# Kernel optimization log

Hardware: AMD Instinct MI355X
Metric: run time of the kernel (lower is better)

Reference implementation:

```python
import jax, jax.numpy as jnp
import numpy as np

EPS = 1e-5
K = 3
N_TAP = K * K


def _bn(x, g, b, m, v):
    # eval-mode batchnorm over channel axis 1 of NCHW
    inv = g / jnp.sqrt(v + EPS)
    return x * inv[None, :, None, None] + (b - m * inv)[None, :, None, None]


def _silu(x):
    return x * jax.nn.sigmoid(x)


def _dcn(x, offset, mask, w, b, pad=1):
    """Modulated deformable conv (DCNv2), stride 1.
    x: [B,C,H,W], offset: [B,2n,H,W] ((dy,dx) per tap), mask: [B,n,H,W],
    w: [O,C,K,K], b: [O]."""
    B, C, H, W = x.shape
    O = w.shape[0]
    ky, kx = jnp.meshgrid(jnp.arange(K), jnp.arange(K), indexing='ij')
    ky = ky.reshape(N_TAP).astype(x.dtype)
    kx = kx.reshape(N_TAP).astype(x.dtype)
    off = offset.reshape(B, N_TAP, 2, H, W)
    base_y = jnp.arange(H, dtype=x.dtype)[None, None, :, None]
    base_x = jnp.arange(W, dtype=x.dtype)[None, None, None, :]
    # fractional sample positions [B,n,H,W]
    py = base_y - pad + ky[None, :, None, None] + off[:, :, 0]
    px = base_x - pad + kx[None, :, None, None] + off[:, :, 1]
    y0 = jnp.floor(py)
    x0 = jnp.floor(px)
    fy = py - y0
    fx = px - x0
    y0i = y0.astype(jnp.int32)
    x0i = x0.astype(jnp.int32)
    x_flat = x.reshape(B, C, 1, H * W)

    def corner(yi, xi, wgt):
        valid = (yi >= 0) & (yi < H) & (xi >= 0) & (xi < W)
        idx = (jnp.clip(yi, 0, H - 1) * W + jnp.clip(xi, 0, W - 1)).reshape(B, 1, N_TAP, H * W)
        v = jnp.take_along_axis(x_flat, idx, axis=-1)  # [B,C,n,HW]
        return v * (wgt * valid.astype(x.dtype)).reshape(B, 1, N_TAP, H * W)

    acc = corner(y0i, x0i, (1 - fy) * (1 - fx))
    acc = acc + corner(y0i, x0i + 1, (1 - fy) * fx)
    acc = acc + corner(y0i + 1, x0i, fy * (1 - fx))
    acc = acc + corner(y0i + 1, x0i + 1, fy * fx)
    val = acc.reshape(B, C, N_TAP, H, W) * mask[:, None]  # modulation
    out = jnp.einsum('bcnhw,ocn->bohw', val, w.reshape(O, C, N_TAP))
    return out + b[None, :, None, None]


def setup_inputs() -> dict:
    key = jax.random.key(0)
    ks = jax.random.split(key, 16)
    B, C1, H, W = 8, 256, 80, 80
    C2 = 256
    Ch = 128  # c_ = int(c2 * 0.5)
    d = {}
    d['x'] = jax.random.normal(ks[0], (B, C1, H, W), jnp.float32)
    # cv1: 1x1 conv (no bias) + BN
    d['cv1_w'] = jax.random.normal(ks[1], (Ch, C1), jnp.float32) * (1.0 / np.sqrt(C1))
    d['bn1_g'] = jax.random.uniform(ks[2], (Ch,), jnp.float32, 0.5, 1.5)
    d['bn1_b'] = jax.random.normal(ks[3], (Ch,), jnp.float32) * 0.1
    d['bn1_m'] = jax.random.normal(ks[4], (Ch,), jnp.float32) * 0.1
    d['bn1_v'] = jax.random.uniform(ks[5], (Ch,), jnp.float32, 0.5, 1.5)
    # offset/mask predictor 3x3 conv (small weights -> modest deformation)
    d['off_w'] = jax.random.normal(ks[6], (3 * N_TAP, Ch, K, K), jnp.float32) * 0.01
    d['off_b'] = jnp.zeros((3 * N_TAP,), jnp.float32)
    # dcn main weight/bias
    d['dcn_w'] = jax.random.normal(ks[7], (Ch, Ch, K, K), jnp.float32) * (1.0 / np.sqrt(Ch * N_TAP))
    d['dcn_b'] = jnp.zeros((Ch,), jnp.float32)
    d['bn2_g'] = jax.random.uniform(ks[8], (Ch,), jnp.float32, 0.5, 1.5)
    d['bn2_b'] = jax.random.normal(ks[9], (Ch,), jnp.float32) * 0.1
    d['bn2_m'] = jax.random.normal(ks[10], (Ch,), jnp.float32) * 0.1
    d['bn2_v'] = jax.random.uniform(ks[11], (Ch,), jnp.float32, 0.5, 1.5)
    # cv2: 1x1 conv (no bias) + BN
    d['cv2_w'] = jax.random.normal(ks[12], (C2, Ch), jnp.float32) * (1.0 / np.sqrt(Ch))
    d['bn3_g'] = jax.random.uniform(ks[13], (C2,), jnp.float32, 0.5, 1.5)
    d['bn3_b'] = jax.random.normal(ks[14], (C2,), jnp.float32) * 0.1
    d['bn3_m'] = jax.random.normal(ks[15], (C2,), jnp.float32) * 0.1
    d['bn3_v'] = jnp.ones((C2,), jnp.float32)
    return d


def reference(x, cv1_w, bn1_g, bn1_b, bn1_m, bn1_v,
              off_w, off_b, dcn_w, dcn_b, bn2_g, bn2_b, bn2_m, bn2_v,
              cv2_w, bn3_g, bn3_b, bn3_m, bn3_v):
    # cv1: 1x1 conv -> BN -> SiLU
    y = _silu(_bn(jnp.einsum('bchw,oc->bohw', x, cv1_w), bn1_g, bn1_b, bn1_m, bn1_v))
    # offset/mask predictor: 3x3 conv, pad 1
    raw = jax.lax.conv_general_dilated(
        y, off_w, window_strides=(1, 1), padding=((1, 1), (1, 1)),
        dimension_numbers=('NCHW', 'OIHW', 'NCHW')) + off_b[None, :, None, None]
    offset = raw[:, :2 * N_TAP]
    mask = jax.nn.sigmoid(raw[:, 2 * N_TAP:])
    # modulated deformable 3x3 conv -> BN -> SiLU
    y = _silu(_bn(_dcn(y, offset, mask, dcn_w, dcn_b), bn2_g, bn2_b, bn2_m, bn2_v))
    # cv2: 1x1 conv -> BN -> SiLU
    y = _silu(_bn(jnp.einsum('bchw,oc->bohw', y, cv2_w), bn3_g, bn3_b, bn3_m, bn3_v))
    return x + y  # shortcut (c1 == c2)
```

## Files before the change

### kernel.cpp

```cpp
#include <hip/hip_runtime.h>
#include <math.h>

#define HWSZ 6400
#define WIMG 80
#define HIMG 80
#define BEPS 1e-5f

typedef __attribute__((ext_vector_type(8))) short short8;
typedef __attribute__((ext_vector_type(4))) float f32x4;

__device__ __forceinline__ unsigned short f2b(float f) {
    unsigned u = __builtin_bit_cast(unsigned, f);
    u += 0x7fffu + ((u >> 16) & 1u);
    return (unsigned short)(u >> 16);
}
__device__ __forceinline__ float b2f(unsigned short h) {
    unsigned u = ((unsigned)h) << 16;
    return __builtin_bit_cast(float, u);
}
__device__ __forceinline__ float silu_f(float t) { return t / (1.f + __expf(-t)); }

#define BPOS(sub, nt, n16, q) (((((sub)*4 + (nt))*16 + (n16))*40) + (q)*8)

__global__ __launch_bounds__(256) void k_prep(
    const float* __restrict__ cv1w, const float* __restrict__ g1, const float* __restrict__ b1,
    const float* __restrict__ m1, const float* __restrict__ v1,
    const float* __restrict__ offw, const float* __restrict__ offb,
    const float* __restrict__ dcnw, const float* __restrict__ dcnb,
    const float* __restrict__ g2, const float* __restrict__ b2,
    const float* __restrict__ m2, const float* __restrict__ v2,
    const float* __restrict__ cv2w, const float* __restrict__ g3, const float* __restrict__ b3,
    const float* __restrict__ m3, const float* __restrict__ v3,
    unsigned short* __restrict__ apk1, unsigned short* __restrict__ apko,
    unsigned short* __restrict__ apkd, unsigned short* __restrict__ apk2,
    float* __restrict__ bias1, float* __restrict__ biaso,
    float* __restrict__ bias2, float* __restrict__ bias3)
{
    int idx = blockIdx.x * 256 + threadIdx.x;
    if (idx < 32768) {
        int j = idx & 7, L = (idx >> 3) & 63, ks = (idx >> 9) & 7, mt = idx >> 12;
        int o = mt * 16 + (L & 15), k = ks * 32 + (L >> 4) * 8 + j;
        float inv = g1[o] * rsqrtf(v1[o] + BEPS);
        apk1[idx] = f2b(cv1w[o * 256 + k] * inv);
    } else if (idx < 69632) {
        int t = idx - 32768;
        int j = t & 7, L = (t >> 3) & 63;
        int mt = t / 18432, rem = t % 18432, ks = rem >> 9;
        int o = mt * 16 + (L & 15);
        int kp = ks * 32 + (L >> 4) * 8 + j;
        int n = kp >> 7, c = kp & 127;
        float wv = (o < 27) ? offw[(size_t)(o * 128 + c) * 9 + n] : 0.f;
        apko[t] = f2b(wv);
    } else if (idx < 217088) {
        int t = idx - 69632;
        int j = t & 7, L = (t >> 3) & 63;
        int mt = t / 18432, rem = t % 18432, ks = rem >> 9;
        int o = mt * 16 + (L & 15);
        int kp = ks * 32 + (L >> 4) * 8 + j;
        int n = kp >> 7, c = kp & 127;
        float inv = g2[o] * rsqrtf(v2[o] + BEPS);
        apkd[t] = f2b(dcnw[(size_t)(o * 128 + c) * 9 + n] * inv);
    } else if (idx < 249856) {
        int t = idx - 217088;
        int j = t & 7, L = (t >> 3) & 63, ks = (t >> 9) & 3, mt = t >> 11;
        int o = mt * 16 + (L & 15), k = ks * 32 + (L >> 4) * 8 + j;
        float inv = g3[o] * rsqrtf(v3[o] + BEPS);
        apk2[t] = f2b(cv2w[o * 128 + k] * inv);
    } else if (idx < 250395) {
        int t = idx - 249856;
        if (t < 128) { float inv = g1[t] * rsqrtf(v1[t] + BEPS); bias1[t] = b1[t] - m1[t] * inv; }
        else if (t < 155) { biaso[t - 128] = offb[t - 128]; }
        else if (t < 283) { int o = t - 155; float inv = g2[o] * rsqrtf(v2[o] + BEPS);
                            bias2[o] = dcnb[o] * inv + b2[o] - m2[o] * inv; }
        else { int o = t - 283; float inv = g3[o] * rsqrtf(v3[o] + BEPS); bias3[o] = b3[o] - m3[o] * inv; }
    }
}

__global__ __launch_bounds__(256) void k_cv1(
    const float* __restrict__ x, const unsigned short* __restrict__ apk1,
    const float* __restrict__ bias1, unsigned short* __restrict__ y1t)
{
    __shared__ __align__(16) unsigned short sB[20480];
    int blk = blockIdx.x;
    int b = blk / 100, pt = blk % 100;
    int p0 = pt * 64;
    int tid = threadIdx.x;
    int lane = tid & 63;
    int w = tid >> 6;
    {
        int px = lane, q = w;
        const float* xb = x + (size_t)b * 256 * HWSZ + p0 + px;
        for (int ks = 0; ks < 8; ++ks) {
            short8 v;
#pragma unroll
            for (int j = 0; j < 8; ++j)
                v[j] = (short)f2b(xb[(size_t)(ks * 32 + q * 8 + j) * HWSZ]);
            *(short8*)&sB[((ks * 4 + (px >> 4)) * 16 + (px & 15)) * 40 + q * 8] = v;
        }
    }
    __syncthreads();
    int n16 = lane & 15, qd = lane >> 4;
    f32x4 acc[2][4];
#pragma unroll
    for (int mi = 0; mi < 2; ++mi)
#pragma unroll
        for (int nt = 0; nt < 4; ++nt) acc[mi][nt] = (f32x4){0.f, 0.f, 0.f, 0.f};
    for (int ks = 0; ks < 8; ++ks) {
        short8 bf[4];
#pragma unroll
        for (int nt = 0; nt < 4; ++nt)
            bf[nt] = *(const short8*)&sB[((ks * 4 + nt) * 16 + n16) * 40 + qd * 8];
#pragma unroll
        for (int mi = 0; mi < 2; ++mi) {
            int mt = w * 2 + mi;
            short8 af = *(const short8*)&apk1[(size_t)((mt * 8 + ks) * 64 + lane) * 8];
#pragma unroll
            for (int nt = 0; nt < 4; ++nt)
                acc[mi][nt] = __builtin_amdgcn_mfma_f32_16x16x32_bf16(af, bf[nt], acc[mi][nt], 0, 0, 0);
        }
    }
    __syncthreads();
#pragma unroll
    for (int mi = 0; mi < 2; ++mi)
#pragma unroll
        for (int nt = 0; nt < 4; ++nt)
#pragma unroll
            for (int r = 0; r < 4; ++r) {
                int o = w * 32 + mi * 16 + qd * 4 + r;
                float sv = silu_f(acc[mi][nt][r] + bias1[o]);
                sB[(nt * 16 + n16) * 136 + o] = f2b(sv);
            }
    __syncthreads();
    {
        int px = tid >> 2, qq = tid & 3;
        unsigned short* ytb = y1t + ((size_t)b * HWSZ + p0 + px) * 128;
#pragma unroll
        for (int seg = 0; seg < 4; ++seg) {
            short8 v = *(const short8*)&sB[px * 136 + qq * 32 + seg * 8];
            *(short8*)&ytb[qq * 32 + seg * 8] = v;
        }
    }
}

__global__ __launch_bounds__(256) void k_off(
    const unsigned short* __restrict__ y1t, const unsigned short* __restrict__ apko,
    const float* __restrict__ biaso, float* __restrict__ raw)
{
    __shared__ __align__(16) unsigned short sV[10240];
    int blk = blockIdx.x;
    int b = blk / 100, pt = blk % 100;
    int p0 = pt * 64;
    int tid = threadIdx.x;
    int lane = tid & 63, w = tid >> 6;
    int n16 = lane & 15, qd = lane >> 4;
    int pxl = tid >> 2, q = tid & 3;
    int p = p0 + pxl;
    int h = p / WIMG, wx = p % WIMG;
    const unsigned short* yb = y1t + (size_t)b * HWSZ * 128;
    f32x4 acc[2];
    acc[0] = (f32x4){0.f, 0.f, 0.f, 0.f};
    acc[1] = (f32x4){0.f, 0.f, 0.f, 0.f};
    const short8 zz = {0, 0, 0, 0, 0, 0, 0, 0};
    for (int n = 0; n < 9; ++n) {
        int hh = h - 1 + n / 3, ww = wx - 1 + n % 3;
        bool valid = ((unsigned)hh < HIMG) && ((unsigned)ww < WIMG);
        int spx = valid ? hh * WIMG + ww : 0;
        const unsigned short* ys = yb + (size_t)spx * 128 + q * 8;
#pragma unroll
        for (int sub = 0; sub < 4; ++sub) {
            short8 v = *(const short8*)&ys[sub * 32];
            if (!valid) v = zz;
            *(short8*)&sV[BPOS(sub, pxl >> 4, pxl & 15, q)] = v;
        }
        __syncthreads();
#pragma unroll
        for (int sub = 0; sub < 4; ++sub) {
            int ks = n * 4 + sub;
            short8 bf = *(const short8*)&sV[BPOS(sub, w, n16, qd)];
#pragma unroll
            for (int mi = 0; mi < 2; ++mi) {
                short8 af = *(const short8*)&apko[(size_t)((mi * 36 + ks) * 64 + lane) * 8];
                acc[mi] = __builtin_amdgcn_mfma_f32_16x16x32_bf16(af, bf, acc[mi], 0, 0, 0);
            }
        }
        __syncthreads();
    }
    float* rb = raw + (size_t)b * 27 * HWSZ + p0 + w * 16 + n16;
#pragma unroll
    for (int mi = 0; mi < 2; ++mi)
#pragma unroll
        for (int r = 0; r < 4; ++r) {
            int o = mi * 16 + qd * 4 + r;
            if (o < 27) {
                float t = acc[mi][r] + biaso[o];
                if (o >= 18) t = 1.f / (1.f + __expf(-t));
                rb[(size_t)o * HWSZ] = t;
            }
        }
}

__global__ __launch_bounds__(256) void k_dcn(
    const unsigned short* __restrict__ y1t, const float* __restrict__ raw,
    const unsigned short* __restrict__ apkd, const float* __restrict__ bias2,
    unsigned short* __restrict__ zt)
{
    __shared__ float swgt[4][9][64];
    __shared__ unsigned short sidx[4][9][64];
    __shared__ __align__(16) unsigned short sV[10240];
    int blk = blockIdx.x;
    int b = blk / 100, pt = blk % 100;
    int p0 = pt * 64;
    int tid = threadIdx.x;

    for (int i = tid; i < 576; i += 256) {
        int n = i / 64, pp = i % 64;
        int p = p0 + pp;
        int h = p / WIMG, wx = p % WIMG;
        const float* rb = raw + (size_t)b * 27 * HWSZ + p;
        float dy = rb[(size_t)(2 * n) * HWSZ];
        float dx = rb[(size_t)(2 * n + 1) * HWSZ];
        float mk = rb[(size_t)(18 + n) * HWSZ];
        float py = (float)(h - 1 + n / 3) + dy;
        float px = (float)(wx - 1 + n % 3) + dx;
        float y0f = floorf(py), x0f = floorf(px);
        float fy = py - y0f, fx = px - x0f;
        int y0 = (int)y0f, x0 = (int)x0f;
#pragma unroll
        for (int k = 0; k < 4; ++k) {
            int yy = y0 + (k >> 1);
            int xx = x0 + (k & 1);
            bool valid = ((unsigned)yy < HIMG) && ((unsigned)xx < WIMG);
            float wk = ((k >> 1) ? fy : 1.f - fy) * ((k & 1) ? fx : 1.f - fx);
            wk = valid ? wk * mk : 0.f;
            int yc = min(max(yy, 0), HIMG - 1);
            int xc = min(max(xx, 0), WIMG - 1);
            sidx[k][n][pp] = (unsigned short)(yc * WIMG + xc);
            swgt[k][n][pp] = wk;
        }
    }
    __syncthreads();

    int lane = tid & 63, w = tid >> 6;
    int n16 = lane & 15, qd = lane >> 4;
    int pxl = tid >> 2, q = tid & 3;
    const unsigned short* yb = y1t + (size_t)b * HWSZ * 128;
    f32x4 acc[2][4];
#pragma unroll
    for (int mi = 0; mi < 2; ++mi)
#pragma unroll
        for (int nt = 0; nt < 4; ++nt) acc[mi][nt] = (f32x4){0.f, 0.f, 0.f, 0.f};

    for (int n = 0; n < 9; ++n) {
        float av[4][8];
#pragma unroll
        for (int sub = 0; sub < 4; ++sub)
#pragma unroll
            for (int j = 0; j < 8; ++j) av[sub][j] = 0.f;
#pragma unroll
        for (int k = 0; k < 4; ++k) {
            float wk = swgt[k][n][pxl];
            const unsigned short* ys = yb + (size_t)sidx[k][n][pxl] * 128 + q * 8;
#pragma unroll
            for (int sub = 0; sub < 4; ++sub) {
                short8 v = *(const short8*)&ys[sub * 32];
#pragma unroll
                for (int j = 0; j < 8; ++j)
                    av[sub][j] = fmaf(wk, b2f((unsigned short)v[j]), av[sub][j]);
            }
        }
#pragma unroll
        for (int sub = 0; sub < 4; ++sub) {
            short8 v;
#pragma unroll
            for (int j = 0; j < 8; ++j) v[j] = (short)f2b(av[sub][j]);
            *(short8*)&sV[BPOS(sub, pxl >> 4, pxl & 15, q)] = v;
        }
        __syncthreads();
#pragma unroll
        for (int sub = 0; sub < 4; ++sub) {
            int ks = n * 4 + sub;
            short8 bf[4];
#pragma unroll
            for (int nt = 0; nt < 4; ++nt)
                bf[nt] = *(const short8*)&sV[BPOS(sub, nt, n16, qd)];
#pragma unroll
            for (int mi = 0; mi < 2; ++mi) {
                short8 af = *(const short8*)&apkd[(size_t)(((2 * w + mi) * 36 + ks) * 64 + lane) * 8];
#pragma unroll
                for (int nt = 0; nt < 4; ++nt)
                    acc[mi][nt] = __builtin_amdgcn_mfma_f32_16x16x32_bf16(af, bf[nt], acc[mi][nt], 0, 0, 0);
            }
        }
        __syncthreads();
    }
#pragma unroll
    for (int mi = 0; mi < 2; ++mi)
#pragma unroll
        for (int nt = 0; nt < 4; ++nt)
#pragma unroll
            for (int r = 0; r < 4; ++r) {
                int o = w * 32 + mi * 16 + qd * 4 + r;
                float sv = silu_f(acc[mi][nt][r] + bias2[o]);
                sV[(nt * 16 + n16) * 136 + o] = f2b(sv);
            }
    __syncthreads();
    {
        int px = tid >> 2, qq = tid & 3;
        unsigned short* zb = zt + ((size_t)b * HWSZ + p0 + px) * 128;
#pragma unroll
        for (int seg = 0; seg < 4; ++seg) {
            short8 v = *(const short8*)&sV[px * 136 + qq * 32 + seg * 8];
            *(short8*)&zb[qq * 32 + seg * 8] = v;
        }
    }
}

__global__ __launch_bounds__(256) void k_cv2(
    const unsigned short* __restrict__ zt, const float* __restrict__ x,
    const unsigned short* __restrict__ apk2, const float* __restrict__ bias3,
    float* __restrict__ out)
{
    int blk = blockIdx.x;
    int b = blk / 100, pt = blk % 100;
    int p0 = pt * 64;
    int tid = threadIdx.x;
    int lane = tid & 63, w = tid >> 6;
    int n16 = lane & 15, qd = lane >> 4;
    const unsigned short* zb = zt + ((size_t)b * HWSZ + p0) * 128;
    f32x4 acc[4][4];
#pragma unroll
    for (int mi = 0; mi < 4; ++mi)
#pragma unroll
        for (int nt = 0; nt < 4; ++nt) acc[mi][nt] = (f32x4){0.f, 0.f, 0.f, 0.f};
#pragma unroll
    for (int ks = 0; ks < 4; ++ks) {
        short8 bf[4];
#pragma unroll
        for (int nt = 0; nt < 4; ++nt)
            bf[nt] = *(const short8*)&zb[(size_t)(nt * 16 + n16) * 128 + ks * 32 + qd * 8];
#pragma unroll
        for (int mi = 0; mi < 4; ++mi) {
            int mt = w * 4 + mi;
            short8 af = *(const short8*)&apk2[(size_t)((mt * 4 + ks) * 64 + lane) * 8];
#pragma unroll
            for (int nt = 0; nt < 4; ++nt)
                acc[mi][nt] = __builtin_amdgcn_mfma_f32_16x16x32_bf16(af, bf[nt], acc[mi][nt], 0, 0, 0);
        }
    }
    const float* xb = x + (size_t)b * 256 * HWSZ;
    float* ob = out + (size_t)b * 256 * HWSZ;
#pragma unroll
    for (int mi = 0; mi < 4; ++mi)
#pragma unroll
        for (int nt = 0; nt < 4; ++nt)
#pragma unroll
            for (int r = 0; r < 4; ++r) {
                int o = w * 64 + mi * 16 + qd * 4 + r;
                size_t idx = (size_t)o * HWSZ + p0 + nt * 16 + n16;
                ob[idx] = xb[idx] + silu_f(acc[mi][nt][r] + bias3[o]);
            }
}

extern "C" void kernel_launch(void* const* d_in, const int* in_sizes, int n_in,
                              void* d_out, int out_size, void* d_ws, size_t ws_size,
                              hipStream_t stream) {
    const float* x     = (const float*)d_in[0];
    const float* cv1w  = (const float*)d_in[1];
    const float* bn1g  = (const float*)d_in[2];
    const float* bn1b  = (const float*)d_in[3];
    const float* bn1m  = (const float*)d_in[4];
    const float* bn1v  = (const float*)d_in[5];
    const float* offw  = (const float*)d_in[6];
    const float* offb  = (const float*)d_in[7];
    const float* dcnw  = (const float*)d_in[8];
    const float* dcnb  = (const float*)d_in[9];
    const float* bn2g  = (const float*)d_in[10];
    const float* bn2b  = (const float*)d_in[11];
    const float* bn2m  = (const float*)d_in[12];
    const float* bn2v  = (const float*)d_in[13];
    const float* cv2w  = (const float*)d_in[14];
    const float* bn3g  = (const float*)d_in[15];
    const float* bn3b  = (const float*)d_in[16];
    const float* bn3m  = (const float*)d_in[17];
    const float* bn3v  = (const float*)d_in[18];
    float* out = (float*)d_out;

    float* base = (float*)d_ws;
    unsigned short* y1t = (unsigned short*)base;
    float* raw   = base + 3276800;
    unsigned short* zt  = (unsigned short*)(base + 4659200);
    unsigned short* apk1 = (unsigned short*)(base + 7936000);
    unsigned short* apko = (unsigned short*)(base + 7952384);
    unsigned short* apkd = (unsigned short*)(base + 7970816);
    unsigned short* apk2 = (unsigned short*)(base + 8044544);
    float* bias1 = base + 8060928;
    float* biaso = base + 8061056;
    float* bias2 = base + 8061088;
    float* bias3 = base + 8061216;

    k_prep<<<979, 256, 0, stream>>>(cv1w, bn1g, bn1b, bn1m, bn1v,
                                    offw, offb, dcnw, dcnb,
                                    bn2g, bn2b, bn2m, bn2v,
                                    cv2w, bn3g, bn3b, bn3m, bn3v,
                                    apk1, apko, apkd, apk2,
                                    bias1, biaso, bias2, bias3);
    k_cv1<<<800, 256, 0, stream>>>(x, apk1, bias1, y1t);
    k_off<<<800, 256, 0, stream>>>(y1t, apko, biaso, raw);
    k_dcn<<<800, 256, 0, stream>>>(y1t, raw, apkd, bias2, zt);
    k_cv2<<<800, 256, 0, stream>>>(zt, x, apk2, bias3, out);
}
```

Before: 235.9 us.

## Stage halo tile in LDS for offset conv; halve DCN tile with double-buffered LDS

The offset-predictor kernel now loads a 226-row halo of y1 into shared memory once and reads all nine taps from it. This replaces nine global gathers and the two barriers per tap. The DCN kernel moves to 32-pixel tiles with 1600 blocks and 8 threads per pixel. It double-buffers the sampled tile in LDS to drop one barrier per tap, and packs bf16 with v_cvt_pk_bf16_f32. In exchange, the offset kernel uses more LDS per block, which may limit occupancy, and DCN weight-fragment loads are repeated across twice as many blocks.

```diff
diff --git a/kernel.cpp b/kernel.cpp
--- a/kernel.cpp
+++ b/kernel.cpp
@@ -8,6 +8,7 @@
 
 typedef __attribute__((ext_vector_type(8))) short short8;
 typedef __attribute__((ext_vector_type(4))) float f32x4;
+typedef __attribute__((ext_vector_type(4))) unsigned u32x4;
 
 __device__ __forceinline__ unsigned short f2b(float f) {
     unsigned u = __builtin_bit_cast(unsigned, f);
@@ -146,44 +147,48 @@
     const unsigned short* __restrict__ y1t, const unsigned short* __restrict__ apko,
     const float* __restrict__ biaso, float* __restrict__ raw)
 {
-    __shared__ __align__(16) unsigned short sV[10240];
+    __shared__ __align__(16) unsigned short sV[227 * 136];
     int blk = blockIdx.x;
     int b = blk / 100, pt = blk % 100;
     int p0 = pt * 64;
     int tid = threadIdx.x;
+    const unsigned short* yb = y1t + (size_t)b * HWSZ * 128;
+    for (int c = tid; c < 226 * 16; c += 256) {
+        int row = c >> 4, col = c & 15;
+        int sp = p0 - 81 + row;
+        sp = min(max(sp, 0), HWSZ - 1);
+        *(short8*)&sV[row * 136 + col * 8] = *(const short8*)&yb[(size_t)sp * 128 + col * 8];
+    }
+    if (tid < 16) {
+        short8 z = {0, 0, 0, 0, 0, 0, 0, 0};
+        *(short8*)&sV[226 * 136 + tid * 8] = z;
+    }
+    __syncthreads();
+
     int lane = tid & 63, w = tid >> 6;
     int n16 = lane & 15, qd = lane >> 4;
-    int pxl = tid >> 2, q = tid & 3;
-    int p = p0 + pxl;
+    int p = p0 + w * 16 + n16;
     int h = p / WIMG, wx = p % WIMG;
-    const unsigned short* yb = y1t + (size_t)b * HWSZ * 128;
     f32x4 acc[2];
     acc[0] = (f32x4){0.f, 0.f, 0.f, 0.f};
     acc[1] = (f32x4){0.f, 0.f, 0.f, 0.f};
-    const short8 zz = {0, 0, 0, 0, 0, 0, 0, 0};
+#pragma unroll
     for (int n = 0; n < 9; ++n) {
-        int hh = h - 1 + n / 3, ww = wx - 1 + n % 3;
+        int dh = n / 3 - 1, dw = n % 3 - 1;
+        int hh = h + dh, ww = wx + dw;
         bool valid = ((unsigned)hh < HIMG) && ((unsigned)ww < WIMG);
-        int spx = valid ? hh * WIMG + ww : 0;
-        const unsigned short* ys = yb + (size_t)spx * 128 + q * 8;
-#pragma unroll
-        for (int sub = 0; sub < 4; ++sub) {
-            short8 v = *(const short8*)&ys[sub * 32];
-            if (!valid) v = zz;
-            *(short8*)&sV[BPOS(sub, pxl >> 4, pxl & 15, q)] = v;
-        }
-        __syncthreads();
-#pragma unroll
-        for (int sub = 0; sub < 4; ++sub) {
-            int ks = n * 4 + sub;
-            short8 bf = *(const short8*)&sV[BPOS(sub, w, n16, qd)];
+        int row = valid ? (81 + w * 16 + n16 + dh * WIMG + dw) : 226;
+        const unsigned short* rV = &sV[row * 136 + qd * 8];
+#pragma unroll
+        for (int s = 0; s < 4; ++s) {
+            int ks = n * 4 + s;
+            short8 bf = *(const short8*)&rV[s * 32];
 #pragma unroll
             for (int mi = 0; mi < 2; ++mi) {
                 short8 af = *(const short8*)&apko[(size_t)((mi * 36 + ks) * 64 + lane) * 8];
                 acc[mi] = __builtin_amdgcn_mfma_f32_16x16x32_bf16(af, bf, acc[mi], 0, 0, 0);
             }
         }
-        __syncthreads();
     }
     float* rb = raw + (size_t)b * 27 * HWSZ + p0 + w * 16 + n16;
 #pragma unroll
@@ -204,16 +209,16 @@
     const unsigned short* __restrict__ apkd, const float* __restrict__ bias2,
     unsigned short* __restrict__ zt)
 {
-    __shared__ float swgt[4][9][64];
-    __shared__ unsigned short sidx[4][9][64];
-    __shared__ __align__(16) unsigned short sV[10240];
+    __shared__ float swgt[4][9][32];
+    __shared__ unsigned short sidx[4][9][32];
+    __shared__ __align__(16) unsigned short sV[2][32 * 136];
     int blk = blockIdx.x;
-    int b = blk / 100, pt = blk % 100;
-    int p0 = pt * 64;
+    int b = blk / 200, pt = blk % 200;
+    int p0 = pt * 32;
     int tid = threadIdx.x;
 
-    for (int i = tid; i < 576; i += 256) {
-        int n = i / 64, pp = i % 64;
+    for (int i = tid; i < 288; i += 256) {
+        int n = i >> 5, pp = i & 31;
         int p = p0 + pp;
         int h = p / WIMG, wx = p % WIMG;
         const float* rb = raw + (size_t)b * 27 * HWSZ + p;
@@ -242,75 +247,81 @@
 
     int lane = tid & 63, w = tid >> 6;
     int n16 = lane & 15, qd = lane >> 4;
-    int pxl = tid >> 2, q = tid & 3;
+    int pxl = tid >> 3, q = tid & 7;
+    int sub = q & 3, qd0 = (q >> 2) * 2;
+    int c0 = sub * 32 + qd0 * 8;
     const unsigned short* yb = y1t + (size_t)b * HWSZ * 128;
-    f32x4 acc[2][4];
+    f32x4 acc[2][2];
 #pragma unroll
     for (int mi = 0; mi < 2; ++mi)
 #pragma unroll
-        for (int nt = 0; nt < 4; ++nt) acc[mi][nt] = (f32x4){0.f, 0.f, 0.f, 0.f};
+        for (int nt = 0; nt < 2; ++nt) acc[mi][nt] = (f32x4){0.f, 0.f, 0.f, 0.f};
 
     for (int n = 0; n < 9; ++n) {
-        float av[4][8];
-#pragma unroll
-        for (int sub = 0; sub < 4; ++sub)
-#pragma unroll
-            for (int j = 0; j < 8; ++j) av[sub][j] = 0.f;
+        float av[16];
+#pragma unroll
+        for (int j = 0; j < 16; ++j) av[j] = 0.f;
 #pragma unroll
         for (int k = 0; k < 4; ++k) {
             float wk = swgt[k][n][pxl];
-            const unsigned short* ys = yb + (size_t)sidx[k][n][pxl] * 128 + q * 8;
-#pragma unroll
-            for (int sub = 0; sub < 4; ++sub) {
-                short8 v = *(const short8*)&ys[sub * 32];
-#pragma unroll
-                for (int j = 0; j < 8; ++j)
-                    av[sub][j] = fmaf(wk, b2f((unsigned short)v[j]), av[sub][j]);
-            }
-        }
-#pragma unroll
-        for (int sub = 0; sub < 4; ++sub) {
-            short8 v;
-#pragma unroll
-            for (int j = 0; j < 8; ++j) v[j] = (short)f2b(av[sub][j]);
-            *(short8*)&sV[BPOS(sub, pxl >> 4, pxl & 15, q)] = v;
+            const unsigned short* ys = yb + (size_t)sidx[k][n][pxl] * 128 + c0;
+            u32x4 u0 = *(const u32x4*)ys;
+            u32x4 u1 = *(const u32x4*)(ys + 8);
+#pragma unroll
+            for (int t = 0; t < 4; ++t) {
+                unsigned ua = u0[t], ub = u1[t];
+                av[2 * t]     = fmaf(wk, __builtin_bit_cast(float, ua << 16), av[2 * t]);
+                av[2 * t + 1] = fmaf(wk, __builtin_bit_cast(float, ua & 0xffff0000u), av[2 * t + 1]);
+                av[8 + 2 * t]     = fmaf(wk, __builtin_bit_cast(float, ub << 16), av[8 + 2 * t]);
+                av[8 + 2 * t + 1] = fmaf(wk, __builtin_bit_cast(float, ub & 0xffff0000u), av[8 + 2 * t + 1]);
+            }
+        }
+        unsigned pk[8];
+#pragma unroll
+        for (int t = 0; t < 8; ++t)
+            asm("v_cvt_pk_bf16_f32 %0, %1, %2" : "=v"(pk[t]) : "v"(av[2 * t]), "v"(av[2 * t + 1]));
+        {
+            unsigned short* dst = &sV[n & 1][pxl * 136 + c0];
+            u32x4 w0 = {pk[0], pk[1], pk[2], pk[3]};
+            u32x4 w1 = {pk[4], pk[5], pk[6], pk[7]};
+            *(u32x4*)dst = w0;
+            *(u32x4*)(dst + 8) = w1;
         }
         __syncthreads();
-#pragma unroll
-        for (int sub = 0; sub < 4; ++sub) {
-            int ks = n * 4 + sub;
-            short8 bf[4];
-#pragma unroll
-            for (int nt = 0; nt < 4; ++nt)
-                bf[nt] = *(const short8*)&sV[BPOS(sub, nt, n16, qd)];
+        const unsigned short* sb = sV[n & 1];
+#pragma unroll
+        for (int s = 0; s < 4; ++s) {
+            int ks = n * 4 + s;
+            short8 bf0 = *(const short8*)&sb[(n16) * 136 + s * 32 + qd * 8];
+            short8 bf1 = *(const short8*)&sb[(16 + n16) * 136 + s * 32 + qd * 8];
 #pragma unroll
             for (int mi = 0; mi < 2; ++mi) {
                 short8 af = *(const short8*)&apkd[(size_t)(((2 * w + mi) * 36 + ks) * 64 + lane) * 8];
-#pragma unroll
-                for (int nt = 0; nt < 4; ++nt)
-                    acc[mi][nt] = __builtin_amdgcn_mfma_f32_16x16x32_bf16(af, bf[nt], acc[mi][nt], 0, 0, 0);
-            }
-        }
-        __syncthreads();
-    }
+                acc[mi][0] = __builtin_amdgcn_mfma_f32_16x16x32_bf16(af, bf0, acc[mi][0], 0, 0, 0);
+                acc[mi][1] = __builtin_amdgcn_mfma_f32_16x16x32_bf16(af, bf1, acc[mi][1], 0, 0, 0);
+            }
+        }
+    }
+    __syncthreads();
+    unsigned short* sE = sV[0];
 #pragma unroll
     for (int mi = 0; mi < 2; ++mi)
 #pragma unroll
-        for (int nt = 0; nt < 4; ++nt)
+        for (int nt = 0; nt < 2; ++nt)
 #pragma unroll
             for (int r = 0; r < 4; ++r) {
                 int o = w * 32 + mi * 16 + qd * 4 + r;
                 float sv = silu_f(acc[mi][nt][r] + bias2[o]);
-                sV[(nt * 16 + n16) * 136 + o] = f2b(sv);
+                sE[(nt * 16 + n16) * 136 + o] = f2b(sv);
             }
     __syncthreads();
     {
-        int px = tid >> 2, qq = tid & 3;
+        int px = tid >> 3, qq = tid & 7;
         unsigned short* zb = zt + ((size_t)b * HWSZ + p0 + px) * 128;
 #pragma unroll
-        for (int seg = 0; seg < 4; ++seg) {
-            short8 v = *(const short8*)&sV[px * 136 + qq * 32 + seg * 8];
-            *(short8*)&zb[qq * 32 + seg * 8] = v;
+        for (int sg = 0; sg < 2; ++sg) {
+            short8 v = *(const short8*)&sE[px * 136 + (qq * 2 + sg) * 8];
+            *(short8*)&zb[(qq * 2 + sg) * 8] = v;
         }
     }
 }
@@ -406,6 +417,6 @@
                                     bias1, biaso, bias2, bias3);
     k_cv1<<<800, 256, 0, stream>>>(x, apk1, bias1, y1t);
     k_off<<<800, 256, 0, stream>>>(y1t, apko, biaso, raw);
-    k_dcn<<<800, 256, 0, stream>>>(y1t, raw, apkd, bias2, zt);
+    k_dcn<<<1600, 256, 0, stream>>>(y1t, raw, apkd, bias2, zt);
     k_cv2<<<800, 256, 0, stream>>>(zt, x, apk2, bias3, out);
 }
```

Measured after the change: 239.4 us. Within noise of the previous version (+1.5%).
